# Kernel optimization log

Hardware: AMD Instinct MI355X
Metric: run time of the kernel (lower is better)

## Reference

```python
import jax, jax.numpy as jnp
import numpy as np
from jax import lax

GROUPS = 4
DILATIONS = (1, 6, 12, 18)
PADDINGS = (1, 6, 12, 18)


def setup_inputs() -> dict:
    key = jax.random.key(0)
    k1, k2, k3 = jax.random.split(key, 3)
    x = jax.random.normal(k1, (8, 64, 320, 320), dtype=jnp.float32)
    weight = jax.random.normal(k2, (64, 16, 3, 3), dtype=jnp.float32) * 0.05
    bias = jax.random.normal(k3, (64,), dtype=jnp.float32) * 0.05
    return {"x": x, "weight": weight, "bias": bias}


def reference(x, weight, bias):
    # x: [b, c, h, w]; channels split into GROUPS groups of c/GROUPS each.
    # Group g is convolved (3x3, stride 1) with dilation DILATIONS[g] and
    # zero-padding PADDINGS[g] (= 'same'), using weight group g of shape
    # [out_ch/GROUPS, c/GROUPS, 3, 3]. Outputs concatenated along channels.
    b, c, h, w = x.shape
    out_ch = weight.shape[0]
    xg = x.reshape(b, GROUPS, c // GROUPS, h, w)
    wg = weight.reshape(GROUPS, out_ch // GROUPS, weight.shape[1], 3, 3)
    dn = lax.conv_dimension_numbers(xg[:, 0].shape, wg[0].shape, ("NCHW", "OIHW", "NCHW"))
    outs = []
    for g in range(GROUPS):
        p, d = PADDINGS[g], DILATIONS[g]
        outs.append(
            lax.conv_general_dilated(
                xg[:, g], wg[g],
                window_strides=(1, 1),
                padding=[(p, p), (p, p)],
                rhs_dilation=(d, d),
                dimension_numbers=dn,
            )
        )
    out = jnp.concatenate(outs, axis=1)  # [b, out_ch, h, w]
    return out + bias[None, :, None, None]
```

## Files before the change

kernel.cpp:

```cpp
#include <hip/hip_runtime.h>
#include <hip/hip_bf16.h>

typedef short short8 __attribute__((ext_vector_type(8)));
typedef short short4_t __attribute__((ext_vector_type(4)));
typedef float floatx4 __attribute__((ext_vector_type(4)));
typedef unsigned short ushort_t;
typedef unsigned int uint32;

#define H 320
#define W 320
#define CG 16
#define NCH 64
#define HW (H * W)
#define CGP 20
#define HALFW 160

__device__ __forceinline__ ushort_t f2bf(float f) {
  unsigned u = __float_as_uint(f);
  return (ushort_t)((u + 0x7FFFu + ((u >> 16) & 1u)) >> 16);
}

__device__ __forceinline__ void barrier_lgkm() {
  asm volatile("s_waitcnt lgkmcnt(0)" ::: "memory");
  __builtin_amdgcn_s_barrier();
}

template<int G>
__device__ __forceinline__ void conv_group(
    const float* __restrict__ x, const float* __restrict__ wgt,
    const float* __restrict__ bias, float* __restrict__ out,
    ushort_t* lds, int b, int bx) {
  constexpr int DIL   = (G == 0) ? 1 : (G == 1) ? 6 : (G == 2) ? 12 : 18;
  constexpr int KOFF  = DIL & 1;
  constexpr int SHIFT = DIL + KOFF;
  constexpr int WH    = (HALFW + 2 * DIL + KOFF + 1) & ~1;
  constexpr int NP    = (WH + 63) / 64;
  constexpr int RPW   = (H + DIL - 1) / DIL;
  constexpr int Q     = (RPW + 3) / 4;
  constexpr int CPW   = (G == 0) ? 12 : (G == 1) ? 2 : 1;
  constexpr int L     = (Q + CPW - 1) / CPW;

  const int tid = threadIdx.x;
  ushort_t* tile = lds;
  ushort_t* swt  = lds + 6 * WH * CGP;
  uint32* swt32  = (uint32*)swt;

#pragma unroll
  for (int k = 0; k < 5; ++k) {
    const int s = tid + k * 256;
    const int jp = s & 3, oc = (s >> 2) & 15, zz = (s >> 6) & 3, t = s >> 8;
    const int tp = 2 * t + (zz >> 1);
    uint32 pk = 0;
    if (tp < 9) {
      const float* wp = wgt + ((size_t)(G * CG + oc) * CG + (zz & 1) * 8 + 2 * jp) * 9 + tp;
      pk = (uint32)f2bf(wp[0]) | ((uint32)f2bf(wp[9]) << 16);
    }
    swt32[s] = pk;
  }
  __syncthreads();

  const int lane = tid & 63;
  const int wv   = tid >> 6;
  const int z = lane >> 4, icq = z & 1, pxl = lane & 15;
  short8 aw[5];
#pragma unroll
  for (int t = 0; t < 5; ++t) aw[t] = *(const short8*)&swt[((t * 4 + z) * 16 + pxl) * 8];
  const float bb = bias[G * CG + pxl];

  const int chunk = bx % CPW;
  const int t1 = bx / CPW;
  const int r  = t1 % DIL;
  const int wb = (t1 / DIL) * HALFW;
  const int q0 = chunk * L;
  const int qend = (q0 + L < Q) ? q0 + L : Q;

  bool zm[NP]; bool inb[NP]; int gofs[NP];
#pragma unroll
  for (int p = 0; p < NP; ++p) {
    const int c = 64 * p + lane;
    inb[p] = (c < WH);
    const int gc = wb + c - SHIFT;
    zm[p] = inb[p] & (gc >= 0) & (gc < W);
    gofs[p] = gc < 0 ? 0 : (gc >= W ? W - 1 : gc);
  }
  const float* chb = x + (size_t)(b * NCH + G * CG + 4 * wv) * HW;

  auto LOADR = [&](int rho, float (&rg)[NP][4]) {
    const int yy = rho * DIL + r;
    const int yyc = yy < 0 ? 0 : (yy >= H ? H - 1 : yy);
    const float* rp = chb + (size_t)yyc * W;
#pragma unroll
    for (int p = 0; p < NP; ++p)
#pragma unroll
      for (int k = 0; k < 4; ++k)
        rg[p][k] = rp[(size_t)k * HW + gofs[p]];
  };

  auto CVTR = [&](int rho, int slot, float (&rg)[NP][4]) {
    const int yy = rho * DIL + r;
    const bool rv = (yy >= 0) & (yy < H);
#pragma unroll
    for (int p = 0; p < NP; ++p) {
      const bool m = rv & zm[p];
      const __hip_bfloat162 h01 = __float22bfloat162_rn(make_float2(rg[p][0], rg[p][1]));
      const __hip_bfloat162 h23 = __float22bfloat162_rn(make_float2(rg[p][2], rg[p][3]));
      uint2 pk;
      pk.x = m ? *(const uint32*)&h01 : 0u;
      pk.y = m ? *(const uint32*)&h23 : 0u;
      if (inb[p]) {
        const int c = 64 * p + lane;
        *(uint2*)&tile[(size_t)(slot * WH + c) * CGP + wv * 4] = pk;
      }
    }
  };

  auto COMPUTE = [&](int q, int m6) {
    const int y = (4 * q + wv) * DIL + r;
    if (y >= H) return;
    const int zh = z >> 1;
    float* outb = out + (size_t)(b * NCH + G * CG + pxl) * HW + (size_t)y * W + wb + 4 * z;
    const ushort_t* rowp[5];
#pragma unroll
    for (int t = 0; t < 5; ++t) {
      const int tp = 2 * t + zh;
      const int ky = tp < 9 ? tp / 3 : 0;
      const int kx = tp < 9 ? tp - ky * 3 : 0;
      int s = m6 + wv + ky; s -= (s >= 6) ? 6 : 0;
      rowp[t] = tile + (size_t)s * (WH * CGP) + (size_t)(pxl + kx * DIL + KOFF) * CGP + icq * 8;
    }
#pragma unroll 2
    for (int ti = 0; ti < HALFW / 16; ++ti) {
      floatx4 acc = {0.f, 0.f, 0.f, 0.f};
#pragma unroll
      for (int t = 0; t < 5; ++t) {
        const ushort_t* pf = rowp[t] + ti * 16 * CGP;
        const short4_t lo = *(const short4_t*)pf;
        const short4_t hi = *(const short4_t*)(pf + 4);
        const short8 bf = {lo[0], lo[1], lo[2], lo[3], hi[0], hi[1], hi[2], hi[3]};
        acc = __builtin_amdgcn_mfma_f32_16x16x32_bf16(bf, aw[t], acc, 0, 0, 0);
      }
      floatx4 st = {acc[0] + bb, acc[1] + bb, acc[2] + bb, acc[3] + bb};
      __builtin_nontemporal_store(st, (floatx4*)(outb + ti * 16));
    }
  };

  auto wrap6 = [](int v) { return v >= 6 ? v - 6 : v; };
  int m6 = (4 * q0 + 5) % 6;

  {
    float ra[NP][4], rb[NP][4];
    LOADR(4 * q0 - 1, ra); LOADR(4 * q0 + 0, rb);
    CVTR(4 * q0 - 1, wrap6(m6 + 0), ra); CVTR(4 * q0 + 0, wrap6(m6 + 1), rb);
    LOADR(4 * q0 + 1, ra); LOADR(4 * q0 + 2, rb);
    CVTR(4 * q0 + 1, wrap6(m6 + 2), ra); CVTR(4 * q0 + 2, wrap6(m6 + 3), rb);
    LOADR(4 * q0 + 3, ra); LOADR(4 * q0 + 4, rb);
    CVTR(4 * q0 + 3, wrap6(m6 + 4), ra); CVTR(4 * q0 + 4, wrap6(m6 + 5), rb);
  }
  barrier_lgkm();

#pragma unroll 1
  for (int q = q0; q < qend - 1; ++q) {
    float ra[NP][4], rb[NP][4], rc[NP][4], rd[NP][4];
    LOADR(4 * q + 5, ra); LOADR(4 * q + 6, rb);
    LOADR(4 * q + 7, rc); LOADR(4 * q + 8, rd);
    COMPUTE(q, m6);
    barrier_lgkm();
    CVTR(4 * q + 5, m6,            ra);
    CVTR(4 * q + 6, wrap6(m6 + 1), rb);
    CVTR(4 * q + 7, wrap6(m6 + 2), rc);
    CVTR(4 * q + 8, wrap6(m6 + 3), rd);
    barrier_lgkm();
    m6 = wrap6(m6 + 4);
  }
  COMPUTE(qend - 1, m6);
}

extern "C" __global__ void __launch_bounds__(256, 3) conv_all(
    const float* __restrict__ x, const float* __restrict__ wgt,
    const float* __restrict__ bias, float* __restrict__ out) {
  extern __shared__ ushort_t lds[];
  const int bid = blockIdx.x;
  const int b = bid & 7;
  const int j = bid >> 3;
  if (j < 36)      conv_group<3>(x, wgt, bias, out, lds, b, j);
  else if (j < 60) conv_group<2>(x, wgt, bias, out, lds, b, j - 36);
  else if (j < 84) conv_group<1>(x, wgt, bias, out, lds, b, j - 60);
  else             conv_group<0>(x, wgt, bias, out, lds, b, j - 84);
}

extern "C" void kernel_launch(void* const* d_in, const int* in_sizes, int n_in,
                              void* d_out, int out_size, void* d_ws, size_t ws_size,
                              hipStream_t stream) {
  const float* x    = (const float*)d_in[0];
  const float* wgt  = (const float*)d_in[1];
  const float* bias = (const float*)d_in[2];
  float* out        = (float*)d_out;

  const size_t lds_bytes = (size_t)(6 * 196 * CGP + 5 * 4 * 16 * 8) * 2;
  conv_all<<<dim3(864), dim3(256), lds_bytes, stream>>>(x, wgt, bias, out);
}
```

Measured before the change: 96.92 us.

## Halve column strip width, double block count, load weights directly to registers

```diff
diff --git a/kernel.cpp b/kernel.cpp
--- a/kernel.cpp
+++ b/kernel.cpp
@@ -13,7 +13,7 @@
 #define NCH 64
 #define HW (H * W)
 #define CGP 20
-#define HALFW 160
+#define SW 80
 
 __device__ __forceinline__ ushort_t f2bf(float f) {
   unsigned u = __float_as_uint(f);
@@ -29,48 +29,39 @@
 __device__ __forceinline__ void conv_group(
     const float* __restrict__ x, const float* __restrict__ wgt,
     const float* __restrict__ bias, float* __restrict__ out,
-    ushort_t* lds, int b, int bx) {
+    ushort_t* tile, int b, int j) {
   constexpr int DIL   = (G == 0) ? 1 : (G == 1) ? 6 : (G == 2) ? 12 : 18;
   constexpr int KOFF  = DIL & 1;
   constexpr int SHIFT = DIL + KOFF;
-  constexpr int WH    = (HALFW + 2 * DIL + KOFF + 1) & ~1;
-  constexpr int NP    = (WH + 63) / 64;
+  constexpr int WH    = (SW + 2 * DIL + KOFF + 1) & ~1;
+  constexpr int NP    = 2;
   constexpr int RPW   = (H + DIL - 1) / DIL;
   constexpr int Q     = (RPW + 3) / 4;
   constexpr int CPW   = (G == 0) ? 12 : (G == 1) ? 2 : 1;
   constexpr int L     = (Q + CPW - 1) / CPW;
 
   const int tid = threadIdx.x;
-  ushort_t* tile = lds;
-  ushort_t* swt  = lds + 6 * WH * CGP;
-  uint32* swt32  = (uint32*)swt;
-
-#pragma unroll
-  for (int k = 0; k < 5; ++k) {
-    const int s = tid + k * 256;
-    const int jp = s & 3, oc = (s >> 2) & 15, zz = (s >> 6) & 3, t = s >> 8;
-    const int tp = 2 * t + (zz >> 1);
-    uint32 pk = 0;
-    if (tp < 9) {
-      const float* wp = wgt + ((size_t)(G * CG + oc) * CG + (zz & 1) * 8 + 2 * jp) * 9 + tp;
-      pk = (uint32)f2bf(wp[0]) | ((uint32)f2bf(wp[9]) << 16);
-    }
-    swt32[s] = pk;
-  }
-  __syncthreads();
-
   const int lane = tid & 63;
   const int wv   = tid >> 6;
-  const int z = lane >> 4, icq = z & 1, pxl = lane & 15;
+  const int z = lane >> 4, icq = z & 1, pxl = lane & 15, zh = z >> 1;
+
   short8 aw[5];
 #pragma unroll
-  for (int t = 0; t < 5; ++t) aw[t] = *(const short8*)&swt[((t * 4 + z) * 16 + pxl) * 8];
+  for (int t = 0; t < 5; ++t) {
+    const int tp = 2 * t + zh;
+#pragma unroll
+    for (int jj = 0; jj < 8; ++jj) {
+      float v = 0.f;
+      if (tp < 9) v = wgt[((size_t)(G * CG + pxl) * CG + icq * 8 + jj) * 9 + tp];
+      aw[t][jj] = (short)f2bf(v);
+    }
+  }
   const float bb = bias[G * CG + pxl];
 
-  const int chunk = bx % CPW;
-  const int t1 = bx / CPW;
+  const int chunk = j % CPW;
+  const int t1 = j / CPW;
   const int r  = t1 % DIL;
-  const int wb = (t1 / DIL) * HALFW;
+  const int wb = (t1 / DIL) * SW;
   const int q0 = chunk * L;
   const int qend = (q0 + L < Q) ? q0 + L : Q;
 
@@ -117,7 +108,6 @@
   auto COMPUTE = [&](int q, int m6) {
     const int y = (4 * q + wv) * DIL + r;
     if (y >= H) return;
-    const int zh = z >> 1;
     float* outb = out + (size_t)(b * NCH + G * CG + pxl) * HW + (size_t)y * W + wb + 4 * z;
     const ushort_t* rowp[5];
 #pragma unroll
@@ -128,8 +118,8 @@
       int s = m6 + wv + ky; s -= (s >= 6) ? 6 : 0;
       rowp[t] = tile + (size_t)s * (WH * CGP) + (size_t)(pxl + kx * DIL + KOFF) * CGP + icq * 8;
     }
-#pragma unroll 2
-    for (int ti = 0; ti < HALFW / 16; ++ti) {
+#pragma unroll
+    for (int ti = 0; ti < SW / 16; ++ti) {
       floatx4 acc = {0.f, 0.f, 0.f, 0.f};
 #pragma unroll
       for (int t = 0; t < 5; ++t) {
@@ -175,17 +165,17 @@
   COMPUTE(qend - 1, m6);
 }
 
-extern "C" __global__ void __launch_bounds__(256, 3) conv_all(
+extern "C" __global__ void __launch_bounds__(256, 5) conv_all(
     const float* __restrict__ x, const float* __restrict__ wgt,
     const float* __restrict__ bias, float* __restrict__ out) {
   extern __shared__ ushort_t lds[];
   const int bid = blockIdx.x;
   const int b = bid & 7;
   const int j = bid >> 3;
-  if (j < 36)      conv_group<3>(x, wgt, bias, out, lds, b, j);
-  else if (j < 60) conv_group<2>(x, wgt, bias, out, lds, b, j - 36);
-  else if (j < 84) conv_group<1>(x, wgt, bias, out, lds, b, j - 60);
-  else             conv_group<0>(x, wgt, bias, out, lds, b, j - 84);
+  if (j < 72)       conv_group<3>(x, wgt, bias, out, lds, b, j);
+  else if (j < 120) conv_group<2>(x, wgt, bias, out, lds, b, j - 72);
+  else if (j < 168) conv_group<1>(x, wgt, bias, out, lds, b, j - 120);
+  else              conv_group<0>(x, wgt, bias, out, lds, b, j - 168);
 }
 
 extern "C" void kernel_launch(void* const* d_in, const int* in_sizes, int n_in,
@@ -196,6 +186,6 @@
   const float* bias = (const float*)d_in[2];
   float* out        = (float*)d_out;
 
-  const size_t lds_bytes = (size_t)(6 * 196 * CGP + 5 * 4 * 16 * 8) * 2;
-  conv_all<<<dim3(864), dim3(256), lds_bytes, stream>>>(x, wgt, bias, out);
+  const size_t lds_bytes = (size_t)6 * 116 * CGP * 2;
+  conv_all<<<dim3(1728), dim3(256), lds_bytes, stream>>>(x, wgt, bias, out);
 }
```

Result: slower. 106.8 us (+10.2%).
